# Performance work log

Hardware: AMD Instinct MI355X
Metric: run time of the kernel (lower is better)

Reference implementation:

```python
import jax, jax.numpy as jnp
import numpy as np

B, N, D, H = 2, 2048, 1024, 16
DH = D // H
SCALE = DH ** -0.5


def setup_inputs() -> dict:
    key = jax.random.key(0)
    ks = jax.random.split(key, 12)
    s = 0.02
    q = jax.random.normal(ks[0], (B, N, D), jnp.float32)
    k = jax.random.normal(ks[1], (B, N, D), jnp.float32)
    v = jax.random.normal(ks[2], (B, N, D), jnp.float32)
    attn_mask = jax.random.randint(ks[3], (B, 1, N, N), 0, 2).astype(bool)
    Wq = jax.random.normal(ks[4], (D, D), jnp.float32) * s
    bq = jnp.zeros((D,), jnp.float32)
    Wk = jax.random.normal(ks[5], (D, D), jnp.float32) * s
    bk = jnp.zeros((D,), jnp.float32)
    Wv = jax.random.normal(ks[6], (D, D), jnp.float32) * s
    bv = jnp.zeros((D,), jnp.float32)
    Wp = jax.random.normal(ks[7], (D, D), jnp.float32) * s
    bp = jnp.zeros((D,), jnp.float32)
    return {"q": q, "k": k, "v": v, "attn_mask": attn_mask,
            "Wq": Wq, "bq": bq, "Wk": Wk, "bk": bk,
            "Wv": Wv, "bv": bv, "Wp": Wp, "bp": bp}


def _heads(x, W, b):
    # (B, N, D) -> (B, H, N, DH)
    Bx, Nx, _ = x.shape
    return (x @ W + b).reshape(Bx, Nx, H, DH).transpose(0, 2, 1, 3)


def reference(q, k, v, attn_mask, Wq, bq, Wk, bk, Wv, bv, Wp, bp):
    qh = _heads(q, Wq, bq)                 # (B, H, Nq, DH)
    kh = _heads(k, Wk, bk)                 # (B, H, Nk, DH)
    vh = _heads(v, Wv, bv)                 # (B, H, Nk, DH)
    attn_raw = jnp.einsum('bhqd,bhkd->bhqk', qh, kh) * SCALE
    attn = jnp.where(attn_mask, -jnp.inf, attn_raw)   # masked_fill(attn_mask, -inf)
    attn = jax.nn.softmax(attn, axis=-1)
    x = jnp.einsum('bhqk,bhkd->bhqd', attn, vh)       # (B, H, Nq, DH)
    x = x.transpose(0, 2, 1, 3).reshape(q.shape[0], q.shape[1], D)
    return x @ Wp + bp
```

## Files before the change

kernel.cpp:

```cpp
#include <hip/hip_runtime.h>
#include <stdint.h>

typedef short bf16x8 __attribute__((ext_vector_type(8)));
typedef float f32x4 __attribute__((ext_vector_type(4)));

#define DEV __device__ __forceinline__

static constexpr int BB = 2, NN = 2048, DD = 1024, HH = 16, DH = 64;
static constexpr float SCLOG2E = 0.18033688011112042f;

static constexpr size_t OFF_PACK   = 1024;
static constexpr size_t PACK_BYTES = (size_t)BB * NN * (NN / 64) * 8ull;
static constexpr size_t OFF_WT     = OFF_PACK + PACK_BYTES;
static constexpr size_t WT_ONE     = (size_t)DD * DD;
static constexpr size_t HEAD_BYTES = (size_t)BB * HH * NN * DH * 2ull;
static constexpr size_t OFF_QH     = OFF_WT + 4 * WT_ONE * 2;
static constexpr size_t OFF_KH     = OFF_QH + HEAD_BYTES;
static constexpr size_t OFF_VT     = OFF_KH + HEAD_BYTES;
static constexpr size_t OFF_X      = OFF_VT + HEAD_BYTES;
static constexpr size_t OFF_KB     = OFF_X + HEAD_BYTES;
static constexpr size_t OFF_VB     = OFF_KB + HEAD_BYTES;
static constexpr size_t NEED_BIG   = OFF_VB + HEAD_BYTES;

DEV unsigned short f2b(float f) {
  unsigned int u = __builtin_bit_cast(unsigned int, f);
  u = (u + 0x7fffu + ((u >> 16) & 1u)) >> 16;
  return (unsigned short)u;
}

#define GLOAD16(gp, lp) __builtin_amdgcn_global_load_lds(                     \
    (const __attribute__((address_space(1))) void*)(gp),                      \
    (__attribute__((address_space(3))) void*)(lp), 16, 0, 0)

__global__ __launch_bounds__(256) void prep(
    const float* W0, const float* W1, const float* W2, const float* W3,
    unsigned short* wt,
    const float* q, const float* k, const float* v,
    unsigned short* qb, unsigned short* kb, unsigned short* vb, int doCvt,
    const void* msrc, unsigned long long* packed) {
  __shared__ unsigned short T[64][72];
  const int id = blockIdx.x, t = threadIdx.x;

  if (id < 1024) {
    int z = id >> 8, local = id & 255;
    int n0 = (local & 15) * 64, k0 = (local >> 4) * 64;
    const float* W = (z == 0) ? W0 : (z == 1) ? W1 : (z == 2) ? W2 : W3;
    unsigned short* dst = wt + (size_t)z * WT_ONE;
    #pragma unroll
    for (int i = 0; i < 4; i++) {
      int row = i * 16 + (t >> 4), col = 4 * (t & 15);
      float4 vv = *(const float4*)&W[(size_t)(k0 + row) * DD + n0 + col];
      T[row][col + 0] = f2b(vv.x); T[row][col + 1] = f2b(vv.y);
      T[row][col + 2] = f2b(vv.z); T[row][col + 3] = f2b(vv.w);
    }
    __syncthreads();
    #pragma unroll
    for (int i = 0; i < 4; i++) {
      int n = i * 16 + (t >> 4), kk = 4 * (t & 15);
      ushort4 o = make_ushort4(T[kk][n], T[kk + 1][n], T[kk + 2][n], T[kk + 3][n]);
      *(ushort4*)&dst[(size_t)(n0 + n) * DD + k0 + kk] = o;
    }
  } else if (id < 7168) {
    if (!doCvt) return;
    int local = id - 1024;
    int z = local / 2048, bx = local % 2048;
    const float* s = (z == 0) ? q : (z == 1) ? k : v;
    unsigned short* d = (z == 0) ? qb : (z == 1) ? kb : vb;
    size_t i = ((size_t)bx * 256 + t) * 8;
    float4 a = *(const float4*)&s[i];
    float4 b2 = *(const float4*)&s[i + 4];
    unsigned short o[8] = {f2b(a.x),  f2b(a.y),  f2b(a.z),  f2b(a.w),
                           f2b(b2.x), f2b(b2.y), f2b(b2.z), f2b(b2.w)};
    *(uint4*)&d[i] = *(const uint4*)o;
  } else {
    unsigned f = 0;
    const unsigned* m32 = (const unsigned*)msrc;
    #pragma unroll
    for (int i = 0; i < 16; i++) {
      unsigned xv = m32[i];
      if (xv != 0u && xv != 1u) f |= 1u;
      if (xv != 0u && xv != 0x3f800000u) f |= 2u;
    }
    int w = (id - 7168) * 256 + t;
    size_t base = (size_t)(w >> 5) * 2048 + (size_t)(w & 31) * 64;
    unsigned long long bits = 0ull;
    if (!(f & 1u)) {
      const int4* p = (const int4*)msrc + (base >> 2);
      #pragma unroll
      for (int c = 0; c < 16; c++) {
        int4 qv = p[c];
        if (qv.x) bits |= 1ull << (4 * c + 0);
        if (qv.y) bits |= 1ull << (4 * c + 1);
        if (qv.z) bits |= 1ull << (4 * c + 2);
        if (qv.w) bits |= 1ull << (4 * c + 3);
      }
    } else if (!(f & 2u)) {
      const float4* p = (const float4*)msrc + (base >> 2);
      #pragma unroll
      for (int c = 0; c < 16; c++) {
        float4 qv = p[c];
        if (qv.x != 0.f) bits |= 1ull << (4 * c + 0);
        if (qv.y != 0.f) bits |= 1ull << (4 * c + 1);
        if (qv.z != 0.f) bits |= 1ull << (4 * c + 2);
        if (qv.w != 0.f) bits |= 1ull << (4 * c + 3);
      }
    } else {
      const uint4* p = (const uint4*)((const char*)msrc + base);
      #pragma unroll
      for (int c = 0; c < 4; c++) {
        uint4 qv = p[c];
        unsigned vals[4] = {qv.x, qv.y, qv.z, qv.w};
        #pragma unroll
        for (int i = 0; i < 4; i++)
          #pragma unroll
          for (int j = 0; j < 4; j++)
            if ((vals[i] >> (8 * j)) & 0xffu) bits |= 1ull << (16 * c + 4 * i + j);
      }
    }
    packed[w] = bits;
  }
}

template <int AFP32>
__global__ __launch_bounds__(256) void gemm_qkv(
    const void* A0, const void* A1, const void* A2,
    const unsigned short* Wt,
    const float* b0, const float* b1, const float* b2,
    unsigned short* dQ, unsigned short* dK, unsigned short* dVt) {
  __shared__ unsigned short Al[2][128 * 32];
  __shared__ unsigned short Bl[2][128 * 32];
  const int t = threadIdx.x, z = blockIdx.z;
  const int m0 = blockIdx.y * 128, n0 = blockIdx.x * 128;
  const unsigned short* Bsrc = Wt + (size_t)z * WT_ONE;
  const void* Av = (z == 0) ? A0 : (z == 1) ? A1 : A2;
  const float* bias = (z == 0) ? b0 : (z == 1) ? b1 : b2;
  const int w = t >> 6, l = t & 63, lr = l & 15, lg = l >> 4;
  const int wm = (w >> 1) * 64, wn = (w & 1) * 64;

  f32x4 acc[4][4];
  #pragma unroll
  for (int i = 0; i < 4; i++)
    #pragma unroll
    for (int j = 0; j < 4; j++) acc[i][j] = (f32x4){0.f, 0.f, 0.f, 0.f};

  for (int k0 = 0; k0 < DD; k0 += 64) {
    __syncthreads();
    if (AFP32) {
      const float* Af = (const float*)Av;
      #pragma unroll
      for (int i = 0; i < 4; i++) {
        int row = i * 32 + (t >> 3), kk = 4 * (t & 7);
        #pragma unroll
        for (int hh = 0; hh < 2; hh++) {
          float4 vv = *(const float4*)&Af[(size_t)(m0 + row) * DD + k0 + hh * 32 + kk];
          ushort4 o4 = make_ushort4(f2b(vv.x), f2b(vv.y), f2b(vv.z), f2b(vv.w));
          *(ushort4*)&Al[hh][row * 32 + kk] = o4;
        }
      }
    } else {
      const unsigned short* Ab = (const unsigned short*)Av;
      #pragma unroll
      for (int p = 0; p < 2; p++)
        #pragma unroll
        for (int c = 0; c < 2; c++)
          GLOAD16(&Ab[(size_t)(m0 + w * 32 + c * 16 + (l >> 2)) * DD + k0 + p * 32 + (l & 3) * 8],
                  &Al[p][(w * 32 + c * 16) * 32]);
    }
    #pragma unroll
    for (int p = 0; p < 2; p++)
      #pragma unroll
      for (int c = 0; c < 2; c++)
        GLOAD16(&Bsrc[(size_t)(n0 + w * 32 + c * 16 + (l >> 2)) * DD + k0 + p * 32 + (l & 3) * 8],
                &Bl[p][(w * 32 + c * 16) * 32]);
    __syncthreads();

    #pragma unroll
    for (int p = 0; p < 2; p++) {
      bf16x8 af[4], bfr[4];
      #pragma unroll
      for (int mi = 0; mi < 4; mi++)
        af[mi] = *(const bf16x8*)&Al[p][(wm + mi * 16 + lr) * 32 + lg * 8];
      #pragma unroll
      for (int ni = 0; ni < 4; ni++)
        bfr[ni] = *(const bf16x8*)&Bl[p][(wn + ni * 16 + lr) * 32 + lg * 8];
      #pragma unroll
      for (int mi = 0; mi < 4; mi++)
        #pragma unroll
        for (int ni = 0; ni < 4; ni++)
          acc[mi][ni] = __builtin_amdgcn_mfma_f32_16x16x32_bf16(
              af[mi], bfr[ni], acc[mi][ni], 0, 0, 0);
    }
  }

  const float scl = (z == 0) ? SCLOG2E : 1.0f;
  #pragma unroll
  for (int mi = 0; mi < 4; mi++) {
    #pragma unroll
    for (int ni = 0; ni < 4; ni++) {
      int col = n0 + wn + ni * 16 + lr;
      float bv = bias[col];
      int h = col >> 6, dh = col & 63;
      int mbase = m0 + wm + mi * 16 + lg * 4;
      if (z == 2) {
        int bq = mbase >> 11, n = mbase & 2047;
        unsigned short o4[4];
        #pragma unroll
        for (int r = 0; r < 4; r++) o4[r] = f2b(acc[mi][ni][r] + bv);
        *(ushort4*)&dVt[(((size_t)(bq * HH + h)) * DH + dh) * NN + n] =
            *(const ushort4*)o4;
      } else {
        unsigned short* dst = (z == 0) ? dQ : dK;
        #pragma unroll
        for (int r = 0; r < 4; r++) {
          int m = mbase + r;
          int bq = m >> 11, n = m & 2047;
          dst[(((size_t)(bq * HH + h)) * NN + n) * DH + dh] =
              f2b((acc[mi][ni][r] + bv) * scl);
        }
      }
    }
  }
}

__global__ __launch_bounds__(256) void gemm_proj(
    const unsigned short* X, const unsigned short* Wt, const float* bias,
    float* out) {
  __shared__ unsigned short Al[2][128 * 32];
  __shared__ unsigned short Bl[2][128 * 32];
  const int t = threadIdx.x;
  const int m0 = blockIdx.y * 128, n0 = blockIdx.x * 128;
  const int w = t >> 6, l = t & 63, lr = l & 15, lg = l >> 4;
  const int wm = (w >> 1) * 64, wn = (w & 1) * 64;

  f32x4 acc[4][4];
  #pragma unroll
  for (int i = 0; i < 4; i++)
    #pragma unroll
    for (int j = 0; j < 4; j++) acc[i][j] = (f32x4){0.f, 0.f, 0.f, 0.f};

  for (int k0 = 0; k0 < DD; k0 += 64) {
    __syncthreads();
    #pragma unroll
    for (int p = 0; p < 2; p++)
      #pragma unroll
      for (int c = 0; c < 2; c++) {
        GLOAD16(&X[(size_t)(m0 + w * 32 + c * 16 + (l >> 2)) * DD + k0 + p * 32 + (l & 3) * 8],
                &Al[p][(w * 32 + c * 16) * 32]);
        GLOAD16(&Wt[(size_t)(n0 + w * 32 + c * 16 + (l >> 2)) * DD + k0 + p * 32 + (l & 3) * 8],
                &Bl[p][(w * 32 + c * 16) * 32]);
      }
    __syncthreads();

    #pragma unroll
    for (int p = 0; p < 2; p++) {
      bf16x8 af[4], bfr[4];
      #pragma unroll
      for (int mi = 0; mi < 4; mi++)
        af[mi] = *(const bf16x8*)&Al[p][(wm + mi * 16 + lr) * 32 + lg * 8];
      #pragma unroll
      for (int ni = 0; ni < 4; ni++)
        bfr[ni] = *(const bf16x8*)&Bl[p][(wn + ni * 16 + lr) * 32 + lg * 8];
      #pragma unroll
      for (int mi = 0; mi < 4; mi++)
        #pragma unroll
        for (int ni = 0; ni < 4; ni++)
          acc[mi][ni] = __builtin_amdgcn_mfma_f32_16x16x32_bf16(
              af[mi], bfr[ni], acc[mi][ni], 0, 0, 0);
    }
  }

  #pragma unroll
  for (int mi = 0; mi < 4; mi++) {
    #pragma unroll
    for (int ni = 0; ni < 4; ni++) {
      int col = n0 + wn + ni * 16 + lr;
      float bv = bias[col];
      #pragma unroll
      for (int r = 0; r < 4; r++) {
        int m = m0 + wm + mi * 16 + lg * 4 + r;
        out[(size_t)m * DD + col] = acc[mi][ni][r] + bv;
      }
    }
  }
}

__global__ __launch_bounds__(256) void attn_k(
    const unsigned short* qh, const unsigned short* kh,
    const unsigned short* vht, const unsigned long long* packed,
    unsigned short* x) {
  __shared__ __align__(16) unsigned short Kl[64 * 64];
  __shared__ __align__(16) unsigned short Vl[64 * 64];
  __shared__ __align__(16) unsigned short Pl[4][16 * 64];
  char* KlB = (char*)Kl;
  char* VlB = (char*)Vl;
  const int t = threadIdx.x, w = t >> 6, l = t & 63;
  const int lr = l & 15, lg = l >> 4;
  char* PlB = (char*)&Pl[w][0];

  const int id = blockIdx.x;
  const int xcd = id & 7, j = id >> 3;
  const int bhg = xcd * 4 + (j >> 5);
  const int q0 = (j & 31) * 64;
  const int b = bhg >> 4, h = bhg & 15;
  const size_t bh = (size_t)b * HH + h;
  const unsigned short* Q = qh + bh * (size_t)NN * DH;
  const unsigned short* K = kh + bh * (size_t)NN * DH;
  const unsigned short* V = vht + bh * (size_t)NN * DH;
  const int qrow = q0 + w * 16 + lr;
  const unsigned long long* pmrow =
      packed + ((size_t)b * NN + qrow) * (NN / 64);

  bf16x8 qf[2];
  #pragma unroll
  for (int kc = 0; kc < 2; kc++)
    qf[kc] = *(const bf16x8*)&Q[(size_t)qrow * DH + kc * 32 + lg * 8];

  f32x4 o[4];
  #pragma unroll
  for (int f = 0; f < 4; f++) o[f] = (f32x4){0.f, 0.f, 0.f, 0.f};
  float lsum = 0.f;

  const int srow = t >> 2, sc0 = (t & 3) * 32;
  const int swr = (srow & 7) << 4;
  const int swl = (lr & 7) << 4;
  const int sA = srow * 128 + (sc0 ^ swr);
  const int sB = srow * 128 + ((sc0 + 16) ^ swr);

  const unsigned short* kpp = &K[(size_t)srow * DH + sc0 / 2];
  const unsigned short* vpp = &V[(size_t)srow * NN + sc0 / 2];
  uint4 k0r = *(const uint4*)kpp, k1r = *(const uint4*)(kpp + 8);
  uint4 v0r = *(const uint4*)vpp, v1r = *(const uint4*)(vpp + 8);

  for (int kt = 0; kt < NN / 64; kt++) {
    __syncthreads();
    *(uint4*)&KlB[sA] = k0r;
    *(uint4*)&KlB[sB] = k1r;
    *(uint4*)&VlB[sA] = v0r;
    *(uint4*)&VlB[sB] = v1r;
    __syncthreads();
    if (kt + 1 < NN / 64) {
      kpp += 64 * DH;
      vpp += 64;
      k0r = *(const uint4*)kpp;  k1r = *(const uint4*)(kpp + 8);
      v0r = *(const uint4*)vpp;  v1r = *(const uint4*)(vpp + 8);
    }

    unsigned long long mw = pmrow[kt];

    f32x4 sv4[4];
    __builtin_amdgcn_s_setprio(1);
    #pragma unroll
    for (int f = 0; f < 4; f++) {
      f32x4 s = (f32x4){0.f, 0.f, 0.f, 0.f};
      bf16x8 kf0 = *(const bf16x8*)&KlB[(16 * f + lr) * 128 + ((lg * 16) ^ swl)];
      bf16x8 kf1 = *(const bf16x8*)&KlB[(16 * f + lr) * 128 + ((64 + lg * 16) ^ swl)];
      s = __builtin_amdgcn_mfma_f32_16x16x32_bf16(kf0, qf[0], s, 0, 0, 0);
      s = __builtin_amdgcn_mfma_f32_16x16x32_bf16(kf1, qf[1], s, 0, 0, 0);
      sv4[f] = s;
    }
    __builtin_amdgcn_s_setprio(0);

    float part = 0.f;
    #pragma unroll
    for (int f = 0; f < 4; f++) {
      unsigned nib = (unsigned)(mw >> (16 * f + 4 * lg)) & 0xFu;
      float pv[4];
      #pragma unroll
      for (int r = 0; r < 4; r++) {
        float s = ((nib >> r) & 1u) ? -30000.f : sv4[f][r];
        pv[r] = __builtin_amdgcn_exp2f(s);
        part += pv[r];
      }
      unsigned w0, w1;
      asm("v_cvt_pk_bf16_f32 %0, %1, %2" : "=v"(w0) : "v"(pv[0]), "v"(pv[1]));
      asm("v_cvt_pk_bf16_f32 %0, %1, %2" : "=v"(w1) : "v"(pv[2]), "v"(pv[3]));
      *(uint2*)&PlB[lr * 128 + ((f * 32 + lg * 8) ^ swl)] = make_uint2(w0, w1);
    }
    lsum += part;
    asm volatile("s_waitcnt lgkmcnt(0)" ::: "memory");
    __builtin_amdgcn_sched_barrier(0);

    bf16x8 pf0 = *(const bf16x8*)&PlB[lr * 128 + ((lg * 16) ^ swl)];
    bf16x8 pf1 = *(const bf16x8*)&PlB[lr * 128 + ((64 + lg * 16) ^ swl)];
    __builtin_amdgcn_s_setprio(1);
    #pragma unroll
    for (int f = 0; f < 4; f++) {
      bf16x8 vf0 = *(const bf16x8*)&VlB[(16 * f + lr) * 128 + ((lg * 16) ^ swl)];
      o[f] = __builtin_amdgcn_mfma_f32_16x16x32_bf16(vf0, pf0, o[f], 0, 0, 0);
      bf16x8 vf1 = *(const bf16x8*)&VlB[(16 * f + lr) * 128 + ((64 + lg * 16) ^ swl)];
      o[f] = __builtin_amdgcn_mfma_f32_16x16x32_bf16(vf1, pf1, o[f], 0, 0, 0);
    }
    __builtin_amdgcn_s_setprio(0);
  }

  lsum += __shfl_xor(lsum, 16);
  lsum += __shfl_xor(lsum, 32);
  float inv = 1.f / fmaxf(lsum, 1e-30f);
  #pragma unroll
  for (int f = 0; f < 4; f++) {
    unsigned w0, w1;
    float a0 = o[f][0] * inv, a1 = o[f][1] * inv;
    float a2 = o[f][2] * inv, a3 = o[f][3] * inv;
    asm("v_cvt_pk_bf16_f32 %0, %1, %2" : "=v"(w0) : "v"(a0), "v"(a1));
    asm("v_cvt_pk_bf16_f32 %0, %1, %2" : "=v"(w1) : "v"(a2), "v"(a3));
    *(uint2*)&x[((size_t)b * NN + qrow) * DD + h * DH + 16 * f + lg * 4] =
        make_uint2(w0, w1);
  }
}

extern "C" void kernel_launch(void* const* d_in, const int* in_sizes, int n_in,
                              void* d_out, int out_size, void* d_ws, size_t ws_size,
                              hipStream_t stream) {
  const float* q  = (const float*)d_in[0];
  const float* k  = (const float*)d_in[1];
  const float* v  = (const float*)d_in[2];
  const void*  mk = d_in[3];
  const float* Wq = (const float*)d_in[4];
  const float* bq = (const float*)d_in[5];
  const float* Wk = (const float*)d_in[6];
  const float* bk = (const float*)d_in[7];
  const float* Wv = (const float*)d_in[8];
  const float* bv = (const float*)d_in[9];
  const float* Wp = (const float*)d_in[10];
  const float* bp = (const float*)d_in[11];
  float* out = (float*)d_out;
  char* ws = (char*)d_ws;

  unsigned long long* packed = (unsigned long long*)(ws + OFF_PACK);
  unsigned short* wt  = (unsigned short*)(ws + OFF_WT);
  unsigned short* qhp = (unsigned short*)(ws + OFF_QH);
  unsigned short* khp = (unsigned short*)(ws + OFF_KH);
  unsigned short* vht = (unsigned short*)(ws + OFF_VT);
  unsigned short* x   = (unsigned short*)(ws + OFF_X);
  unsigned short* qb  = (unsigned short*)(ws + OFF_X);
  unsigned short* kb  = (unsigned short*)(ws + OFF_KB);
  unsigned short* vb  = (unsigned short*)(ws + OFF_VB);

  const bool big = ws_size >= NEED_BIG;

  prep<<<dim3(7680), 256, 0, stream>>>(Wq, Wk, Wv, Wp, wt, q, k, v,
                                       qb, kb, vb, big ? 1 : 0, mk, packed);
  if (big) {
    gemm_qkv<0><<<dim3(8, 32, 3), 256, 0, stream>>>(qb, kb, vb, wt, bq, bk, bv,
                                                    qhp, khp, vht);
  } else {
    gemm_qkv<1><<<dim3(8, 32, 3), 256, 0, stream>>>(q, k, v, wt, bq, bk, bv,
                                                    qhp, khp, vht);
  }
  attn_k<<<dim3(1024), 256, 0, stream>>>(qhp, khp, vht, packed, x);
  gemm_proj<<<dim3(8, 32), 256, 0, stream>>>(x, wt + 3 * WT_ONE, bp, out);
}
```

Before: 170.4 us.

## Software-pipeline bf16 GEMMs with async LDS prefetch and chunked block remap

Replaces the bf16-input QKV and projection GEMMs with one templated kernel. It double-buffers 32-wide K stages, issuing the next stage's global-to-LDS loads before computing the current one, and uses explicit vmcnt waits with raw barriers. Block indices are remapped into row-chunks spread across the XCD-style chunk index to improve L2 locality, and the QKV launch becomes a flat 1D grid. The fp32 fallback path is simplified to a single-buffered 32-wide loop. This adds more barriers per K step, and correctness relies on the hand-placed waitcnt.

```diff
diff --git a/kernel.cpp b/kernel.cpp
--- a/kernel.cpp
+++ b/kernel.cpp
@@ -121,18 +121,118 @@
   }
 }
 
-template <int AFP32>
-__global__ __launch_bounds__(256) void gemm_qkv(
-    const void* A0, const void* A1, const void* A2,
+template <int PROJ>
+__global__ __launch_bounds__(256) void gemm_pl(
+    const unsigned short* A0, const unsigned short* A1,
+    const unsigned short* A2, const unsigned short* Wt,
+    const float* b0, const float* b1, const float* b2, const float* b3,
+    unsigned short* dQ, unsigned short* dK, unsigned short* dVt, float* out) {
+  __shared__ unsigned short Al[2][128 * 32];
+  __shared__ unsigned short Bl[2][128 * 32];
+  const int t = threadIdx.x;
+  const int w = t >> 6, l = t & 63, lr = l & 15, lg = l >> 4;
+  const int wm = (w >> 1) * 64, wn = (w & 1) * 64;
+
+  const int wg = blockIdx.x;
+  const int chunk = wg & 7, local = wg >> 3;
+  const int colBlk = local >> 2, rowBlk = chunk * 4 + (local & 3);
+  const int m0 = rowBlk * 128, n0 = colBlk * 128;
+  const int z = PROJ ? 3 : (n0 >> 10);
+  const int n0z = PROJ ? n0 : (n0 & 1023);
+  const unsigned short* Asrc = PROJ ? A0 : (z == 0 ? A0 : (z == 1 ? A1 : A2));
+  const unsigned short* Bsrc = Wt + (size_t)z * WT_ONE;
+  const float* bias = PROJ ? b3 : (z == 0 ? b0 : (z == 1 ? b1 : b2));
+
+  const unsigned short* aP =
+      Asrc + (size_t)(m0 + w * 32 + (l >> 2)) * DD + (l & 3) * 8;
+  const unsigned short* bP =
+      Bsrc + (size_t)(n0z + w * 32 + (l >> 2)) * DD + (l & 3) * 8;
+
+  f32x4 acc[4][4];
+  #pragma unroll
+  for (int i = 0; i < 4; i++)
+    #pragma unroll
+    for (int j = 0; j < 4; j++) acc[i][j] = (f32x4){0.f, 0.f, 0.f, 0.f};
+
+  auto STAGE = [&](int k0, int buf) {
+    GLOAD16(aP + k0,           &Al[buf][(w * 32) * 32]);
+    GLOAD16(aP + k0 + 16 * DD, &Al[buf][(w * 32 + 16) * 32]);
+    GLOAD16(bP + k0,           &Bl[buf][(w * 32) * 32]);
+    GLOAD16(bP + k0 + 16 * DD, &Bl[buf][(w * 32 + 16) * 32]);
+  };
+
+  STAGE(0, 0);
+  for (int it = 0; it < DD / 32; ++it) {
+    if (it + 1 < DD / 32) {
+      STAGE((it + 1) * 32, (it + 1) & 1);
+      asm volatile("s_waitcnt vmcnt(4)" ::: "memory");
+    } else {
+      asm volatile("s_waitcnt vmcnt(0)" ::: "memory");
+    }
+    __builtin_amdgcn_s_barrier();
+
+    const int buf = it & 1;
+    bf16x8 af[4], bfr[4];
+    #pragma unroll
+    for (int mi = 0; mi < 4; mi++)
+      af[mi] = *(const bf16x8*)&Al[buf][(wm + mi * 16 + lr) * 32 + lg * 8];
+    #pragma unroll
+    for (int ni = 0; ni < 4; ni++)
+      bfr[ni] = *(const bf16x8*)&Bl[buf][(wn + ni * 16 + lr) * 32 + lg * 8];
+    #pragma unroll
+    for (int mi = 0; mi < 4; mi++)
+      #pragma unroll
+      for (int ni = 0; ni < 4; ni++)
+        acc[mi][ni] = __builtin_amdgcn_mfma_f32_16x16x32_bf16(
+            af[mi], bfr[ni], acc[mi][ni], 0, 0, 0);
+    __builtin_amdgcn_s_barrier();
+  }
+
+  const float scl = (!PROJ && z == 0) ? SCLOG2E : 1.0f;
+  #pragma unroll
+  for (int mi = 0; mi < 4; mi++) {
+    #pragma unroll
+    for (int ni = 0; ni < 4; ni++) {
+      int col = n0z + wn + ni * 16 + lr;
+      float bv = bias[col];
+      int h = col >> 6, dh = col & 63;
+      int mbase = m0 + wm + mi * 16 + lg * 4;
+      if (PROJ) {
+        #pragma unroll
+        for (int r = 0; r < 4; r++)
+          out[(size_t)(mbase + r) * DD + col] = acc[mi][ni][r] + bv;
+      } else if (z == 2) {
+        int bq = mbase >> 11, n = mbase & 2047;
+        unsigned short o4[4];
+        #pragma unroll
+        for (int r = 0; r < 4; r++) o4[r] = f2b(acc[mi][ni][r] + bv);
+        *(ushort4*)&dVt[(((size_t)(bq * HH + h)) * DH + dh) * NN + n] =
+            *(const ushort4*)o4;
+      } else {
+        unsigned short* dst = (z == 0) ? dQ : dK;
+        #pragma unroll
+        for (int r = 0; r < 4; r++) {
+          int m = mbase + r;
+          int bq = m >> 11, n = m & 2047;
+          dst[(((size_t)(bq * HH + h)) * NN + n) * DH + dh] =
+              f2b((acc[mi][ni][r] + bv) * scl);
+        }
+      }
+    }
+  }
+}
+
+__global__ __launch_bounds__(256) void gemm_qkv_f32(
+    const float* A0, const float* A1, const float* A2,
     const unsigned short* Wt,
     const float* b0, const float* b1, const float* b2,
     unsigned short* dQ, unsigned short* dK, unsigned short* dVt) {
-  __shared__ unsigned short Al[2][128 * 32];
-  __shared__ unsigned short Bl[2][128 * 32];
+  __shared__ unsigned short Al[128 * 32];
+  __shared__ unsigned short Bl[128 * 32];
   const int t = threadIdx.x, z = blockIdx.z;
   const int m0 = blockIdx.y * 128, n0 = blockIdx.x * 128;
   const unsigned short* Bsrc = Wt + (size_t)z * WT_ONE;
-  const void* Av = (z == 0) ? A0 : (z == 1) ? A1 : A2;
+  const float* Af = (z == 0) ? A0 : (z == 1) ? A1 : A2;
   const float* bias = (z == 0) ? b0 : (z == 1) ? b1 : b2;
   const int w = t >> 6, l = t & 63, lr = l & 15, lg = l >> 4;
   const int wm = (w >> 1) * 64, wn = (w & 1) * 64;
@@ -143,53 +243,34 @@
     #pragma unroll
     for (int j = 0; j < 4; j++) acc[i][j] = (f32x4){0.f, 0.f, 0.f, 0.f};
 
-  for (int k0 = 0; k0 < DD; k0 += 64) {
+  for (int k0 = 0; k0 < DD; k0 += 32) {
     __syncthreads();
-    if (AFP32) {
-      const float* Af = (const float*)Av;
-      #pragma unroll
-      for (int i = 0; i < 4; i++) {
-        int row = i * 32 + (t >> 3), kk = 4 * (t & 7);
-        #pragma unroll
-        for (int hh = 0; hh < 2; hh++) {
-          float4 vv = *(const float4*)&Af[(size_t)(m0 + row) * DD + k0 + hh * 32 + kk];
-          ushort4 o4 = make_ushort4(f2b(vv.x), f2b(vv.y), f2b(vv.z), f2b(vv.w));
-          *(ushort4*)&Al[hh][row * 32 + kk] = o4;
-        }
-      }
-    } else {
-      const unsigned short* Ab = (const unsigned short*)Av;
-      #pragma unroll
-      for (int p = 0; p < 2; p++)
-        #pragma unroll
-        for (int c = 0; c < 2; c++)
-          GLOAD16(&Ab[(size_t)(m0 + w * 32 + c * 16 + (l >> 2)) * DD + k0 + p * 32 + (l & 3) * 8],
-                  &Al[p][(w * 32 + c * 16) * 32]);
-    }
-    #pragma unroll
-    for (int p = 0; p < 2; p++)
-      #pragma unroll
-      for (int c = 0; c < 2; c++)
-        GLOAD16(&Bsrc[(size_t)(n0 + w * 32 + c * 16 + (l >> 2)) * DD + k0 + p * 32 + (l & 3) * 8],
-                &Bl[p][(w * 32 + c * 16) * 32]);
+    #pragma unroll
+    for (int i = 0; i < 4; i++) {
+      int row = i * 32 + (t >> 3), kk = 4 * (t & 7);
+      float4 vv = *(const float4*)&Af[(size_t)(m0 + row) * DD + k0 + kk];
+      ushort4 o4 = make_ushort4(f2b(vv.x), f2b(vv.y), f2b(vv.z), f2b(vv.w));
+      *(ushort4*)&Al[row * 32 + kk] = o4;
+    }
+    #pragma unroll
+    for (int c = 0; c < 2; c++)
+      GLOAD16(&Bsrc[(size_t)(n0 + w * 32 + c * 16 + (l >> 2)) * DD + k0 + (l & 3) * 8],
+              &Bl[(w * 32 + c * 16) * 32]);
     __syncthreads();
 
-    #pragma unroll
-    for (int p = 0; p < 2; p++) {
-      bf16x8 af[4], bfr[4];
-      #pragma unroll
-      for (int mi = 0; mi < 4; mi++)
-        af[mi] = *(const bf16x8*)&Al[p][(wm + mi * 16 + lr) * 32 + lg * 8];
+    bf16x8 af[4], bfr[4];
+    #pragma unroll
+    for (int mi = 0; mi < 4; mi++)
+      af[mi] = *(const bf16x8*)&Al[(wm + mi * 16 + lr) * 32 + lg * 8];
+    #pragma unroll
+    for (int ni = 0; ni < 4; ni++)
+      bfr[ni] = *(const bf16x8*)&Bl[(wn + ni * 16 + lr) * 32 + lg * 8];
+    #pragma unroll
+    for (int mi = 0; mi < 4; mi++)
       #pragma unroll
       for (int ni = 0; ni < 4; ni++)
-        bfr[ni] = *(const bf16x8*)&Bl[p][(wn + ni * 16 + lr) * 32 + lg * 8];
-      #pragma unroll
-      for (int mi = 0; mi < 4; mi++)
-        #pragma unroll
-        for (int ni = 0; ni < 4; ni++)
-          acc[mi][ni] = __builtin_amdgcn_mfma_f32_16x16x32_bf16(
-              af[mi], bfr[ni], acc[mi][ni], 0, 0, 0);
-    }
+        acc[mi][ni] = __builtin_amdgcn_mfma_f32_16x16x32_bf16(
+            af[mi], bfr[ni], acc[mi][ni], 0, 0, 0);
   }
 
   const float scl = (z == 0) ? SCLOG2E : 1.0f;
@@ -217,68 +298,6 @@
           dst[(((size_t)(bq * HH + h)) * NN + n) * DH + dh] =
               f2b((acc[mi][ni][r] + bv) * scl);
         }
-      }
-    }
-  }
-}
-
-__global__ __launch_bounds__(256) void gemm_proj(
-    const unsigned short* X, const unsigned short* Wt, const float* bias,
-    float* out) {
-  __shared__ unsigned short Al[2][128 * 32];
-  __shared__ unsigned short Bl[2][128 * 32];
-  const int t = threadIdx.x;
-  const int m0 = blockIdx.y * 128, n0 = blockIdx.x * 128;
-  const int w = t >> 6, l = t & 63, lr = l & 15, lg = l >> 4;
-  const int wm = (w >> 1) * 64, wn = (w & 1) * 64;
-
-  f32x4 acc[4][4];
-  #pragma unroll
-  for (int i = 0; i < 4; i++)
-    #pragma unroll
-    for (int j = 0; j < 4; j++) acc[i][j] = (f32x4){0.f, 0.f, 0.f, 0.f};
-
-  for (int k0 = 0; k0 < DD; k0 += 64) {
-    __syncthreads();
-    #pragma unroll
-    for (int p = 0; p < 2; p++)
-      #pragma unroll
-      for (int c = 0; c < 2; c++) {
-        GLOAD16(&X[(size_t)(m0 + w * 32 + c * 16 + (l >> 2)) * DD + k0 + p * 32 + (l & 3) * 8],
-                &Al[p][(w * 32 + c * 16) * 32]);
-        GLOAD16(&Wt[(size_t)(n0 + w * 32 + c * 16 + (l >> 2)) * DD + k0 + p * 32 + (l & 3) * 8],
-                &Bl[p][(w * 32 + c * 16) * 32]);
-      }
-    __syncthreads();
-
-    #pragma unroll
-    for (int p = 0; p < 2; p++) {
-      bf16x8 af[4], bfr[4];
-      #pragma unroll
-      for (int mi = 0; mi < 4; mi++)
-        af[mi] = *(const bf16x8*)&Al[p][(wm + mi * 16 + lr) * 32 + lg * 8];
-      #pragma unroll
-      for (int ni = 0; ni < 4; ni++)
-        bfr[ni] = *(const bf16x8*)&Bl[p][(wn + ni * 16 + lr) * 32 + lg * 8];
-      #pragma unroll
-      for (int mi = 0; mi < 4; mi++)
-        #pragma unroll
-        for (int ni = 0; ni < 4; ni++)
-          acc[mi][ni] = __builtin_amdgcn_mfma_f32_16x16x32_bf16(
-              af[mi], bfr[ni], acc[mi][ni], 0, 0, 0);
-    }
-  }
-
-  #pragma unroll
-  for (int mi = 0; mi < 4; mi++) {
-    #pragma unroll
-    for (int ni = 0; ni < 4; ni++) {
-      int col = n0 + wn + ni * 16 + lr;
-      float bv = bias[col];
-      #pragma unroll
-      for (int r = 0; r < 4; r++) {
-        int m = m0 + wm + mi * 16 + lg * 4 + r;
-        out[(size_t)m * DD + col] = acc[mi][ni][r] + bv;
       }
     }
   }
@@ -441,12 +460,15 @@
   prep<<<dim3(7680), 256, 0, stream>>>(Wq, Wk, Wv, Wp, wt, q, k, v,
                                        qb, kb, vb, big ? 1 : 0, mk, packed);
   if (big) {
-    gemm_qkv<0><<<dim3(8, 32, 3), 256, 0, stream>>>(qb, kb, vb, wt, bq, bk, bv,
-                                                    qhp, khp, vht);
+    gemm_pl<0><<<dim3(768), 256, 0, stream>>>(qb, kb, vb, wt,
+                                              bq, bk, bv, bp,
+                                              qhp, khp, vht, nullptr);
   } else {
-    gemm_qkv<1><<<dim3(8, 32, 3), 256, 0, stream>>>(q, k, v, wt, bq, bk, bv,
-                                                    qhp, khp, vht);
+    gemm_qkv_f32<<<dim3(8, 32, 3), 256, 0, stream>>>(q, k, v, wt, bq, bk, bv,
+                                                     qhp, khp, vht);
   }
   attn_k<<<dim3(1024), 256, 0, stream>>>(qhp, khp, vht, packed, x);
-  gemm_proj<<<dim3(8, 32), 256, 0, stream>>>(x, wt + 3 * WT_ONE, bp, out);
-}
+  gemm_pl<1><<<dim3(256), 256, 0, stream>>>(x, nullptr, nullptr, wt,
+                                            bq, bk, bv, bp,
+                                            nullptr, nullptr, nullptr, out);
+}
```

Measured after the change: 163.0 us (median of 3 runs). 4.3% less time.
